# Kernel tuning notes

Measured on AMD Instinct MI355X. Metric: run time of the kernel, lower is better.

The kernel has to match this reference:

```python
import jax, jax.numpy as jnp
import numpy as np
from jax import lax

K = 3  # kernel size
PAD = K // 2


def _patches(x):
    # x: [B,C,H,W] -> [B,C,K*K,H,W] (zero-padded 'same' neighborhoods)
    B, C, H, W = x.shape
    xp = jnp.pad(x, ((0, 0), (0, 0), (PAD, PAD), (PAD, PAD)))
    ps = [xp[:, :, i:i + H, j:j + W] for i in range(K) for j in range(K)]
    return jnp.stack(ps, axis=2)


def pac_conv2d(x, guide, w, b):
    # Pixel-adaptive conv (pacnet, kernel_type='gaussian', not channel-wise).
    # adaptive kernel from guidance: exp(-0.5 * ||g_patch - g_center||^2)
    gp = _patches(guide)                      # [B,C,P,H,W]
    d2 = jnp.sum((gp - guide[:, :, None]) ** 2, axis=1)  # [B,P,H,W]
    kern = jnp.exp(-0.5 * d2)                 # [B,P,H,W]
    xp = _patches(x)                          # [B,Cin,P,H,W]
    wf = w.reshape(w.shape[0], w.shape[1], K * K)  # [Cout,Cin,P]
    out = jnp.einsum('bcphw,bphw,ocp->bohw', xp, kern, wf)
    return out + b[None, :, None, None]


def conv2d(x, w, b):
    out = lax.conv_general_dilated(x, w, (1, 1), 'SAME',
                                   dimension_numbers=('NCHW', 'OIHW', 'NCHW'))
    return out + b[None, :, None, None]


def setup_inputs() -> dict:
    key = jax.random.key(0)
    ks = jax.random.split(key, 10)
    B, C, H, W = 8, 64, 128, 128
    fan = C * K * K
    s = 1.0 / np.sqrt(fan)
    inp = {
        'x': jax.random.normal(ks[0], (B, C, H, W), jnp.float32),
        'edge': jax.random.normal(ks[1], (B, C, H, W), jnp.float32),
        'w_pac1': jax.random.normal(ks[2], (C, C, K, K), jnp.float32) * s,
        'b_pac1': jax.random.normal(ks[3], (C,), jnp.float32) * s,
        'w_pac2': jax.random.normal(ks[4], (C, C, K, K), jnp.float32) * s,
        'b_pac2': jax.random.normal(ks[5], (C,), jnp.float32) * s,
        'w_e1': jax.random.normal(ks[6], (C, C, K, K), jnp.float32) * s,
        'b_e1': jax.random.normal(ks[7], (C,), jnp.float32) * s,
        'w_e2': jax.random.normal(ks[8], (C, C, K, K), jnp.float32) * s,
        'b_e2': jax.random.normal(ks[9], (C,), jnp.float32) * s,
    }
    return inp


def reference(x, edge, w_pac1, b_pac1, w_pac2, b_pac2, w_e1, b_e1, w_e2, b_e2):
    res_scale = 1.0
    # i=0: pac conv on sr (guided by current edge), plain conv on edge
    res_sr = pac_conv2d(x, edge, w_pac1, b_pac1)
    res_edge = conv2d(edge, w_e1, b_e1)
    # i=1: activation on both
    res_sr = jax.nn.relu(res_sr)
    res_edge = jax.nn.relu(res_edge)
    # i=2: pac conv guided by updated edge, plain conv on edge
    res_sr = pac_conv2d(res_sr, res_edge, w_pac2, b_pac2)
    res_edge = conv2d(res_edge, w_e2, b_e2)
    # dual residual
    res_sr = x + res_sr * res_scale
    res_edge = edge + res_edge * res_scale
    return (res_sr, res_edge)
```

## Files before the change

### kernel.cpp

```cpp
#include <hip/hip_runtime.h>

typedef unsigned short u16;
typedef __attribute__((ext_vector_type(8))) short s8;
typedef __attribute__((ext_vector_type(4))) float f4;

#define B_  8
#define C_  64
#define H_  128
#define W_  128
#define HW_ (H_*W_)
#define PITCH 72
#define WSZ 36864


static __device__ __forceinline__ u16 f2bu(float f) {
    union { float f; unsigned u; } c; c.f = f;
    unsigned u = c.u;
    u += 0x7fffu + ((u >> 16) & 1u);
    return (u16)(u >> 16);
}
static __device__ __forceinline__ float bu2f(u16 u) {
    union { unsigned u; float f; } c; c.u = ((unsigned)u) << 16; return c.f;
}

__global__ __launch_bounds__(256) void transpose2(
    const float* __restrict__ x, const float* __restrict__ edge,
    u16* __restrict__ x_t, u16* __restrict__ edge_t)
{
    __shared__ float s[16][68];
    const int t  = threadIdx.x;
    const int h  = blockIdx.x >> 3;
    const int w0 = (blockIdx.x & 7) * 16;
    const int b  = blockIdx.y;
    const float* src = blockIdx.z ? edge : x;
    u16* dst = blockIdx.z ? edge_t : x_t;
    {
        int c = t >> 2, wq = t & 3;
        float4 v = *(const float4*)(src + ((size_t)b*C_ + c)*HW_ + h*W_ + w0 + wq*4);
        s[wq*4+0][c] = v.x; s[wq*4+1][c] = v.y; s[wq*4+2][c] = v.z; s[wq*4+3][c] = v.w;
    }
    __syncthreads();
    {
        int w = t >> 4, cg = t & 15;
        float4 v = *(const float4*)(&s[w][cg*4]);
        ushort4 o; o.x = f2bu(v.x); o.y = f2bu(v.y); o.z = f2bu(v.z); o.w = f2bu(v.w);
        *(ushort4*)(dst + ((size_t)b*HW_ + h*W_ + w0 + w)*64 + cg*4) = o;
    }
}

__global__ __launch_bounds__(256) void wt_all(
    const float* __restrict__ w0, const float* __restrict__ w1,
    const float* __restrict__ w2, const float* __restrict__ w3,
    u16* __restrict__ dst)
{
    int idx = blockIdx.x*256 + threadIdx.x;
    int cid = blockIdx.y;
    const float* w = (cid == 0) ? w0 : (cid == 1) ? w1 : (cid == 2) ? w2 : w3;
    int p = idx >> 12, o = (idx >> 6) & 63, c = idx & 63;
    dst[(size_t)cid*WSZ + idx] = f2bu(w[((size_t)o*64 + c)*9 + p]);
}

static __device__ __forceinline__ void stage_tile(
    u16* __restrict__ s_t, const u16* __restrict__ src, int b, int th0, int tw0, int t)
{
    for (int i = t; i < 10*18*8; i += 256) {
        int pix = i >> 3, ch = i & 7;
        int rr = pix / 18, ww = pix - rr*18;
        int gr = th0 + rr - 1, gw = tw0 + ww - 1;
        uint4 v = {0u,0u,0u,0u};
        if ((unsigned)gr < (unsigned)H_ && (unsigned)gw < (unsigned)W_)
            v = *(const uint4*)(src + ((size_t)b*HW_ + gr*W_ + gw)*64 + ch*8);
        *(uint4*)(&s_t[pix*PITCH + ch*8]) = v;
    }
}

template<bool PAC>
static __device__ __forceinline__ void conv_core(
    const u16* __restrict__ s_t, const float* __restrict__ s_k,
    const u16* __restrict__ w, const float* __restrict__ bias,
    f4 acc[2][4], int wvM, int wvN, int ln, int quad)
{
#pragma unroll
    for (int mf = 0; mf < 2; ++mf) {
        f4 bv;
#pragma unroll
        for (int r = 0; r < 4; ++r) bv[r] = bias[wvM*32 + mf*16 + quad*4 + r];
#pragma unroll
        for (int nf = 0; nf < 4; ++nf) acc[mf][nf] = bv;
    }

#pragma unroll
    for (int p = 0; p < 9; ++p) {
        const int dr = p / 3, dc = p - dr*3;
        s8 a[2][2];
#pragma unroll
        for (int mf = 0; mf < 2; ++mf)
#pragma unroll
            for (int kc = 0; kc < 2; ++kc)
                a[mf][kc] = *(const s8*)(w + (((size_t)p*64 + wvM*32 + mf*16 + ln)*64 + kc*32 + quad*8));
        s8 bfr[4][2];
#pragma unroll
        for (int nf = 0; nf < 4; ++nf) {
            const u16* base = &s_t[((wvN*4 + nf + dr)*18 + ln + dc)*PITCH];
#pragma unroll
            for (int kc = 0; kc < 2; ++kc)
                bfr[nf][kc] = *(const s8*)(base + kc*32 + quad*8);
        }
        if (PAC) {
            float kv[4];
#pragma unroll
            for (int nf = 0; nf < 4; ++nf)
                kv[nf] = s_k[p*128 + (wvN*4 + nf)*16 + ln];
#pragma unroll
            for (int mf = 0; mf < 2; ++mf)
#pragma unroll
                for (int nf = 0; nf < 4; ++nf) {
                    f4 d = {0.f, 0.f, 0.f, 0.f};
                    d = __builtin_amdgcn_mfma_f32_16x16x32_bf16(a[mf][0], bfr[nf][0], d, 0, 0, 0);
                    d = __builtin_amdgcn_mfma_f32_16x16x32_bf16(a[mf][1], bfr[nf][1], d, 0, 0, 0);
                    acc[mf][nf] += kv[nf] * d;
                }
        } else {
#pragma unroll
            for (int mf = 0; mf < 2; ++mf)
#pragma unroll
                for (int nf = 0; nf < 4; ++nf) {
                    acc[mf][nf] = __builtin_amdgcn_mfma_f32_16x16x32_bf16(a[mf][0], bfr[nf][0], acc[mf][nf], 0, 0, 0);
                    acc[mf][nf] = __builtin_amdgcn_mfma_f32_16x16x32_bf16(a[mf][1], bfr[nf][1], acc[mf][nf], 0, 0, 0);
                }
        }
    }
}

static __device__ __forceinline__ void store_t(
    u16* __restrict__ out, f4 acc[2][4], int b, int th0, int tw0,
    int wvM, int wvN, int ln, int quad)
{
#pragma unroll
    for (int mf = 0; mf < 2; ++mf)
#pragma unroll
        for (int nf = 0; nf < 4; ++nf) {
            f4 v = acc[mf][nf];
            ushort4 o;
            o.x = f2bu(fmaxf(v[0], 0.f)); o.y = f2bu(fmaxf(v[1], 0.f));
            o.z = f2bu(fmaxf(v[2], 0.f)); o.w = f2bu(fmaxf(v[3], 0.f));
            size_t pix = (size_t)b*HW_ + (th0 + wvN*4 + nf)*W_ + tw0 + ln;
            *(ushort4*)(out + pix*64 + wvM*32 + mf*16 + quad*4) = o;
        }
}

static __device__ __forceinline__ void store_f(
    float* __restrict__ out, const u16* __restrict__ resid_t,
    f4 acc[2][4], int b, int th0, int tw0, int wvM, int wvN, int ln, int quad)
{
#pragma unroll
    for (int mf = 0; mf < 2; ++mf)
#pragma unroll
        for (int nf = 0; nf < 4; ++nf) {
            size_t pix = (size_t)b*HW_ + (th0 + wvN*4 + nf)*W_ + tw0 + ln;
            ushort4 rv = *(const ushort4*)(resid_t + pix*64 + wvM*32 + mf*16 + quad*4);
            float rr[4] = {bu2f(rv.x), bu2f(rv.y), bu2f(rv.z), bu2f(rv.w)};
#pragma unroll
            for (int r = 0; r < 4; ++r) {
                int och = wvM*32 + mf*16 + quad*4 + r;
                out[((size_t)b*C_ + och)*HW_ + (th0 + wvN*4 + nf)*W_ + tw0 + ln]
                    = acc[mf][nf][r] + rr[r];
            }
        }
}

template<bool STAGE1>
__global__ __launch_bounds__(256, 2) void fused_stage(
    const u16* __restrict__ inA_t, const u16* __restrict__ inB_t,
    const u16* __restrict__ wA, const u16* __restrict__ wB,
    const float* __restrict__ biasA, const float* __restrict__ biasB,
    const u16* __restrict__ residA_t, const u16* __restrict__ residB_t,
    u16* __restrict__ outA_t, u16* __restrict__ outB_t,
    float* __restrict__ outA_f, float* __restrict__ outB_f)
{
    __shared__ u16   s_t[10*18*PITCH];
    __shared__ float s_k[9*128];

    const int t    = threadIdx.x;
    const int b    = blockIdx.y;
    const int th0  = (blockIdx.x >> 3) * 8;
    const int tw0  = (blockIdx.x & 7) * 16;
    const int wv   = t >> 6;
    const int wvM  = wv >> 1;
    const int wvN  = wv & 1;
    const int lane = t & 63;
    const int ln   = lane & 15;
    const int quad = lane >> 4;

    stage_tile(s_t, inA_t, b, th0, tw0, t);
    __syncthreads();

    {
        const int px   = t & 127;
        const int half = t >> 7;
        const int p0   = half ? 5 : 0;
        const int np   = half ? 4 : 5;
        const int py   = px >> 4, pxc = px & 15;
        float d2[5];
#pragma unroll
        for (int k = 0; k < 5; ++k) d2[k] = 0.f;
        const u16* cb = &s_t[((py+1)*18 + (pxc+1))*PITCH];
#pragma unroll 1
        for (int co = 0; co < 8; ++co) {
            s8 c8 = *(const s8*)(cb + co*8);
            float cf[8];
#pragma unroll
            for (int j = 0; j < 8; ++j) cf[j] = bu2f((u16)c8[j]);
#pragma unroll
            for (int k = 0; k < 5; ++k) {
                if (k < np) {
                    int p = p0 + k;
                    int dr = p / 3, dc = p - dr*3;
                    s8 n8 = *(const s8*)(&s_t[((py + dr)*18 + pxc + dc)*PITCH + co*8]);
#pragma unroll
                    for (int j = 0; j < 8; ++j) {
                        float d = bu2f((u16)n8[j]) - cf[j];
                        d2[k] += d * d;
                    }
                }
            }
        }
#pragma unroll
        for (int k = 0; k < 5; ++k)
            if (k < np) s_k[(p0+k)*128 + px] = __expf(-0.5f * d2[k]);
    }

    {
        f4 acc[2][4];
        conv_core<false>(s_t, nullptr, wA, biasA, acc, wvM, wvN, ln, quad);
        if (STAGE1) store_t(outA_t, acc, b, th0, tw0, wvM, wvN, ln, quad);
        else        store_f(outA_f, residA_t, acc, b, th0, tw0, wvM, wvN, ln, quad);
    }

    __syncthreads();
    stage_tile(s_t, inB_t, b, th0, tw0, t);
    __syncthreads();

    {
        f4 acc[2][4];
        conv_core<true>(s_t, s_k, wB, biasB, acc, wvM, wvN, ln, quad);
        if (STAGE1) store_t(outB_t, acc, b, th0, tw0, wvM, wvN, ln, quad);
        else        store_f(outB_f, residB_t, acc, b, th0, tw0, wvM, wvN, ln, quad);
    }
}

extern "C" void kernel_launch(void* const* d_in, const int* in_sizes, int n_in,
                              void* d_out, int out_size, void* d_ws, size_t ws_size,
                              hipStream_t stream)
{
    const float* x      = (const float*)d_in[0];
    const float* edge   = (const float*)d_in[1];
    const float* w_pac1 = (const float*)d_in[2];
    const float* b_pac1 = (const float*)d_in[3];
    const float* w_pac2 = (const float*)d_in[4];
    const float* b_pac2 = (const float*)d_in[5];
    const float* w_e1   = (const float*)d_in[6];
    const float* b_e1   = (const float*)d_in[7];
    const float* w_e2   = (const float*)d_in[8];
    const float* b_e2   = (const float*)d_in[9];

    float* out_sr   = (float*)d_out;
    float* out_edge = out_sr + (size_t)B_*C_*HW_;

    const size_t NT = (size_t)B_*HW_*64;
    u16* x_t         = (u16*)d_ws;
    u16* edge_t      = x_t + NT;
    u16* res_edge1_t = edge_t + NT;
    u16* res_sr1_t   = res_edge1_t + NT;
    u16* w_t         = res_sr1_t + NT;

    dim3 blk(256);

    transpose2<<<dim3(H_*8, B_, 2), blk, 0, stream>>>(x, edge, x_t, edge_t);
    wt_all<<<dim3(144, 4), blk, 0, stream>>>(w_e1, w_pac1, w_e2, w_pac2, w_t);

    fused_stage<true ><<<dim3(128, B_), blk, 0, stream>>>(
        edge_t, x_t, w_t + 0*WSZ, w_t + 1*WSZ, b_e1, b_pac1,
        nullptr, nullptr, res_edge1_t, res_sr1_t, nullptr, nullptr);
    fused_stage<false><<<dim3(128, B_), blk, 0, stream>>>(
        res_edge1_t, res_sr1_t, w_t + 2*WSZ, w_t + 3*WSZ, b_e2, b_pac2,
        edge_t, x_t, nullptr, nullptr, out_edge, out_sr);
}
```

Measured before the change: 238.9 us.

## Fuse NCHW-to-NHWC bf16 transpose into stage-1 tile staging, read fp32 residuals directly

Drops the separate transpose kernel. Stage 1 now loads fp32 NCHW tiles straight from the inputs, converts them to bf16 and writes them to shared memory in channel-last layout. Stage 2 adds the residual from the original fp32 inputs instead of from the bf16 transposed copies. This removes a kernel launch and a full write and re-read of two transposed tensors, and makes the residual exact fp32. The cost is strided per-channel global loads and 4-byte scattered LDS writes inside the conv kernel, which may stage less efficiently than the old vectorized path.

```diff
diff --git a/kernel.cpp b/kernel.cpp
--- a/kernel.cpp
+++ b/kernel.cpp
@@ -21,31 +21,6 @@
 }
 static __device__ __forceinline__ float bu2f(u16 u) {
     union { unsigned u; float f; } c; c.u = ((unsigned)u) << 16; return c.f;
-}
-
-__global__ __launch_bounds__(256) void transpose2(
-    const float* __restrict__ x, const float* __restrict__ edge,
-    u16* __restrict__ x_t, u16* __restrict__ edge_t)
-{
-    __shared__ float s[16][68];
-    const int t  = threadIdx.x;
-    const int h  = blockIdx.x >> 3;
-    const int w0 = (blockIdx.x & 7) * 16;
-    const int b  = blockIdx.y;
-    const float* src = blockIdx.z ? edge : x;
-    u16* dst = blockIdx.z ? edge_t : x_t;
-    {
-        int c = t >> 2, wq = t & 3;
-        float4 v = *(const float4*)(src + ((size_t)b*C_ + c)*HW_ + h*W_ + w0 + wq*4);
-        s[wq*4+0][c] = v.x; s[wq*4+1][c] = v.y; s[wq*4+2][c] = v.z; s[wq*4+3][c] = v.w;
-    }
-    __syncthreads();
-    {
-        int w = t >> 4, cg = t & 15;
-        float4 v = *(const float4*)(&s[w][cg*4]);
-        ushort4 o; o.x = f2bu(v.x); o.y = f2bu(v.y); o.z = f2bu(v.z); o.w = f2bu(v.w);
-        *(ushort4*)(dst + ((size_t)b*HW_ + h*W_ + w0 + w)*64 + cg*4) = o;
-    }
 }
 
 __global__ __launch_bounds__(256) void wt_all(
@@ -74,6 +49,40 @@
     }
 }
 
+static __device__ __forceinline__ void stage_tile_f32(
+    u16* __restrict__ s_t, const float* __restrict__ src, int b, int th0, int tw0, int t)
+{
+    const bool lok = (tw0 != 0);
+    const bool rok = (tw0 != W_ - 16);
+    for (int i = t; i < 320; i += 256) {
+        const int cp = i & 31, rr = i >> 5;
+        const int gr = th0 + rr - 1;
+        const int c0 = cp * 2;
+        float v0[18], v1[18];
+        if ((unsigned)gr < (unsigned)H_) {
+            const float* a0 = src + ((size_t)b*C_ + c0)*HW_ + (size_t)gr*W_ + tw0;
+            const float* a1 = a0 + HW_;
+            v0[0]  = lok ? a0[-1] : 0.f;
+            v1[0]  = lok ? a1[-1] : 0.f;
+#pragma unroll
+            for (int g = 0; g < 4; ++g) {
+                *(f4*)(v0 + 1 + g*4) = *(const f4*)(a0 + g*4);
+                *(f4*)(v1 + 1 + g*4) = *(const f4*)(a1 + g*4);
+            }
+            v0[17] = rok ? a0[16] : 0.f;
+            v1[17] = rok ? a1[16] : 0.f;
+        } else {
+#pragma unroll
+            for (int j = 0; j < 18; ++j) { v0[j] = 0.f; v1[j] = 0.f; }
+        }
+#pragma unroll
+        for (int j = 0; j < 18; ++j) {
+            unsigned pk = (unsigned)f2bu(v0[j]) | ((unsigned)f2bu(v1[j]) << 16);
+            *(unsigned*)(&s_t[(rr*18 + j)*PITCH + c0]) = pk;
+        }
+    }
+}
+
 template<bool PAC>
 static __device__ __forceinline__ void conv_core(
     const u16* __restrict__ s_t, const float* __restrict__ s_k,
@@ -150,31 +159,29 @@
 }
 
 static __device__ __forceinline__ void store_f(
-    float* __restrict__ out, const u16* __restrict__ resid_t,
+    float* __restrict__ out, const float* __restrict__ resid,
     f4 acc[2][4], int b, int th0, int tw0, int wvM, int wvN, int ln, int quad)
 {
 #pragma unroll
     for (int mf = 0; mf < 2; ++mf)
 #pragma unroll
         for (int nf = 0; nf < 4; ++nf) {
-            size_t pix = (size_t)b*HW_ + (th0 + wvN*4 + nf)*W_ + tw0 + ln;
-            ushort4 rv = *(const ushort4*)(resid_t + pix*64 + wvM*32 + mf*16 + quad*4);
-            float rr[4] = {bu2f(rv.x), bu2f(rv.y), bu2f(rv.z), bu2f(rv.w)};
 #pragma unroll
             for (int r = 0; r < 4; ++r) {
                 int och = wvM*32 + mf*16 + quad*4 + r;
-                out[((size_t)b*C_ + och)*HW_ + (th0 + wvN*4 + nf)*W_ + tw0 + ln]
-                    = acc[mf][nf][r] + rr[r];
+                size_t idx = ((size_t)b*C_ + och)*HW_ + (th0 + wvN*4 + nf)*W_ + tw0 + ln;
+                out[idx] = acc[mf][nf][r] + resid[idx];
             }
         }
 }
 
 template<bool STAGE1>
 __global__ __launch_bounds__(256, 2) void fused_stage(
+    const float* __restrict__ inA_f, const float* __restrict__ inB_f,
     const u16* __restrict__ inA_t, const u16* __restrict__ inB_t,
     const u16* __restrict__ wA, const u16* __restrict__ wB,
     const float* __restrict__ biasA, const float* __restrict__ biasB,
-    const u16* __restrict__ residA_t, const u16* __restrict__ residB_t,
+    const float* __restrict__ residA_f, const float* __restrict__ residB_f,
     u16* __restrict__ outA_t, u16* __restrict__ outB_t,
     float* __restrict__ outA_f, float* __restrict__ outB_f)
 {
@@ -192,7 +199,8 @@
     const int ln   = lane & 15;
     const int quad = lane >> 4;
 
-    stage_tile(s_t, inA_t, b, th0, tw0, t);
+    if (STAGE1) stage_tile_f32(s_t, inA_f, b, th0, tw0, t);
+    else        stage_tile    (s_t, inA_t, b, th0, tw0, t);
     __syncthreads();
 
     {
@@ -234,18 +242,19 @@
         f4 acc[2][4];
         conv_core<false>(s_t, nullptr, wA, biasA, acc, wvM, wvN, ln, quad);
         if (STAGE1) store_t(outA_t, acc, b, th0, tw0, wvM, wvN, ln, quad);
-        else        store_f(outA_f, residA_t, acc, b, th0, tw0, wvM, wvN, ln, quad);
+        else        store_f(outA_f, residA_f, acc, b, th0, tw0, wvM, wvN, ln, quad);
     }
 
     __syncthreads();
-    stage_tile(s_t, inB_t, b, th0, tw0, t);
+    if (STAGE1) stage_tile_f32(s_t, inB_f, b, th0, tw0, t);
+    else        stage_tile    (s_t, inB_t, b, th0, tw0, t);
     __syncthreads();
 
     {
         f4 acc[2][4];
         conv_core<true>(s_t, s_k, wB, biasB, acc, wvM, wvN, ln, quad);
         if (STAGE1) store_t(outB_t, acc, b, th0, tw0, wvM, wvN, ln, quad);
-        else        store_f(outB_f, residB_t, acc, b, th0, tw0, wvM, wvN, ln, quad);
+        else        store_f(outB_f, residB_f, acc, b, th0, tw0, wvM, wvN, ln, quad);
     }
 }
 
@@ -268,21 +277,20 @@
     float* out_edge = out_sr + (size_t)B_*C_*HW_;
 
     const size_t NT = (size_t)B_*HW_*64;
-    u16* x_t         = (u16*)d_ws;
-    u16* edge_t      = x_t + NT;
-    u16* res_edge1_t = edge_t + NT;
+    u16* res_edge1_t = (u16*)d_ws;
     u16* res_sr1_t   = res_edge1_t + NT;
     u16* w_t         = res_sr1_t + NT;
 
     dim3 blk(256);
 
-    transpose2<<<dim3(H_*8, B_, 2), blk, 0, stream>>>(x, edge, x_t, edge_t);
     wt_all<<<dim3(144, 4), blk, 0, stream>>>(w_e1, w_pac1, w_e2, w_pac2, w_t);
 
     fused_stage<true ><<<dim3(128, B_), blk, 0, stream>>>(
-        edge_t, x_t, w_t + 0*WSZ, w_t + 1*WSZ, b_e1, b_pac1,
+        edge, x, nullptr, nullptr,
+        w_t + 0*WSZ, w_t + 1*WSZ, b_e1, b_pac1,
         nullptr, nullptr, res_edge1_t, res_sr1_t, nullptr, nullptr);
     fused_stage<false><<<dim3(128, B_), blk, 0, stream>>>(
-        res_edge1_t, res_sr1_t, w_t + 2*WSZ, w_t + 3*WSZ, b_e2, b_pac2,
-        edge_t, x_t, nullptr, nullptr, out_edge, out_sr);
-}
+        nullptr, nullptr, res_edge1_t, res_sr1_t,
+        w_t + 2*WSZ, w_t + 3*WSZ, b_e2, b_pac2,
+        edge, x, nullptr, nullptr, out_edge, out_sr);
+}
```

After: 245.7 us. +2.8%, slower.
